# Kernel optimization log

Measured on AMD Instinct MI355X. Metric: run time of the kernel, lower is better.

## Reference

```python
import jax, jax.numpy as jnp
import numpy as np


def _skew(v):
    # v: [B,3] -> [B,3,3] skew-symmetric matrices
    z = jnp.zeros_like(v[:, 0])
    return jnp.stack([
        jnp.stack([z, -v[:, 2], v[:, 1]], axis=-1),
        jnp.stack([v[:, 2], z, -v[:, 0]], axis=-1),
        jnp.stack([-v[:, 1], v[:, 0], z], axis=-1),
    ], axis=-2)


def _so3_exp(phi):
    # phi: [B,3] -> [B,3,3] rotation matrices via Rodrigues formula
    theta_sq = jnp.sum(phi * phi, axis=-1)            # [B]
    small = theta_sq < 1e-8
    theta_sq_safe = jnp.where(small, 1.0, theta_sq)
    theta = jnp.sqrt(theta_sq_safe)
    A = jnp.where(small, 1.0 - theta_sq / 6.0, jnp.sin(theta) / theta)
    Bc = jnp.where(small, 0.5 - theta_sq / 24.0, (1.0 - jnp.cos(theta)) / theta_sq_safe)
    K = _skew(phi)                                    # [B,3,3]
    I = jnp.eye(3, dtype=phi.dtype)
    return I + A[:, None, None] * K + Bc[:, None, None] * (K @ K)


def setup_inputs() -> dict:
    key = jax.random.key(0)
    k1, = jax.random.split(key, 1)
    B, T = 4096, 1024
    imu = jax.random.normal(k1, (B, 6, T), dtype=jnp.float32) * 0.5  # gyro + accel
    t = jnp.broadcast_to(jnp.arange(T, dtype=jnp.float32) * 0.005, (B, T))  # 200 Hz
    x = jnp.concatenate([t[:, None, :], imu], axis=1)  # [B,7,T]
    return {"x": x}


def reference(x) -> jnp.ndarray:
    # x: [B,7,T] -> y: [B,15] = [DC (9), DV (3), DR (3)] per window
    Bn = x.shape[0]
    t = x[:, 0, :]                          # [B,T]
    dt = (t[:, 1:] - t[:, :-1]).T           # [T-1,B]
    w = jnp.moveaxis(x[:, 1:4, :-1], 2, 0)  # [T-1,B,3] gyro at idx-1
    a = jnp.moveaxis(x[:, 4:7, :-1], 2, 0)  # [T-1,B,3] accel at idx-1

    DC0 = jnp.broadcast_to(jnp.eye(3, dtype=x.dtype), (Bn, 3, 3))
    DV0 = jnp.zeros((Bn, 3), dtype=x.dtype)
    DR0 = jnp.zeros((Bn, 3), dtype=x.dtype)

    def step(carry, inp):
        DC, DV, DR = carry
        dt_k, w_k, a_k = inp                         # [B], [B,3], [B,3]
        dtc = dt_k[:, None]
        DCa = jnp.einsum('bij,bj->bi', DC, a_k)      # [B,3]
        DR = DR + DV * dtc + 0.5 * DCa * dtc * dtc
        DV = DV + DCa * dtc
        DC = DC @ _so3_exp(w_k * dtc)
        return (DC, DV, DR), None

    (DC, DV, DR), _ = jax.lax.scan(step, (DC0, DV0, DR0), (dt, w, a))
    return jnp.concatenate([DC.reshape(Bn, 9), DV, DR], axis=-1)  # [B,15]
```

## Files before the change

kernel.cpp:

```cpp
#include <hip/hip_runtime.h>

#define T_LEN 1024
#define NSTEP 1023

__device__ __forceinline__ void so3_exp(float px, float py, float pz, float R[9]) {
    float t2 = px * px + py * py + pz * pz;
    float A, Bc;
    if (t2 < 1e-2f) {
        float t4 = t2 * t2;
        A  = 1.0f - t2 * (1.0f / 6.0f)  + t4 * (1.0f / 120.0f);
        Bc = 0.5f - t2 * (1.0f / 24.0f) + t4 * (1.0f / 720.0f);
    } else {
        float th = sqrtf(t2);
        A = __sinf(th) / th;
        float sh = __sinf(0.5f * th);
        Bc = 2.0f * sh * sh / t2;
    }
    float xx = px * px, yy = py * py, zz = pz * pz;
    float xy = px * py, xz = px * pz, yz = py * pz;
    R[0] = 1.0f - Bc * (yy + zz);
    R[1] = Bc * xy - A * pz;
    R[2] = Bc * xz + A * py;
    R[3] = Bc * xy + A * pz;
    R[4] = 1.0f - Bc * (xx + zz);
    R[5] = Bc * yz - A * px;
    R[6] = Bc * xz - A * py;
    R[7] = Bc * yz + A * px;
    R[8] = 1.0f - Bc * (xx + yy);
}

extern "C" __global__ void __launch_bounds__(256)
rmi_kernel(const float* __restrict__ x, float* __restrict__ out) {
    const int b   = blockIdx.x;
    const int tid = threadIdx.x;
    const float* __restrict__ xb = x + (size_t)b * (7 * T_LEN);

    __shared__ float s[256 * 17];

    const int k0 = tid * 4;
    float4 t4  = *reinterpret_cast<const float4*>(xb + k0);
    float  tn  = (k0 + 4 < T_LEN) ? xb[k0 + 4] : 0.0f;
    float4 wx4 = *reinterpret_cast<const float4*>(xb + 1 * T_LEN + k0);
    float4 wy4 = *reinterpret_cast<const float4*>(xb + 2 * T_LEN + k0);
    float4 wz4 = *reinterpret_cast<const float4*>(xb + 3 * T_LEN + k0);
    float4 ax4 = *reinterpret_cast<const float4*>(xb + 4 * T_LEN + k0);
    float4 ay4 = *reinterpret_cast<const float4*>(xb + 5 * T_LEN + k0);
    float4 az4 = *reinterpret_cast<const float4*>(xb + 6 * T_LEN + k0);

    float tv[5]  = {t4.x, t4.y, t4.z, t4.w, tn};
    float wxv[4] = {wx4.x, wx4.y, wx4.z, wx4.w};
    float wyv[4] = {wy4.x, wy4.y, wy4.z, wy4.w};
    float wzv[4] = {wz4.x, wz4.y, wz4.z, wz4.w};
    float axv[4] = {ax4.x, ax4.y, ax4.z, ax4.w};
    float ayv[4] = {ay4.x, ay4.y, ay4.z, ay4.w};
    float azv[4] = {az4.x, az4.y, az4.z, az4.w};

    float C0 = 1.f, C1 = 0.f, C2 = 0.f;
    float C3 = 0.f, C4 = 1.f, C5 = 0.f;
    float C6 = 0.f, C7 = 0.f, C8 = 1.f;
    float V0 = 0.f, V1 = 0.f, V2 = 0.f;
    float R0 = 0.f, R1 = 0.f, R2 = 0.f;
    float tau = 0.f;

#pragma unroll
    for (int j = 0; j < 4; ++j) {
        int k = k0 + j;
        if (k < NSTEP) {
            float dt = tv[j + 1] - tv[j];
            float ax = axv[j], ay = ayv[j], az = azv[j];
            float Ca0 = C0 * ax + C1 * ay + C2 * az;
            float Ca1 = C3 * ax + C4 * ay + C5 * az;
            float Ca2 = C6 * ax + C7 * ay + C8 * az;
            float h = 0.5f * dt * dt;
            R0 += V0 * dt + Ca0 * h;
            R1 += V1 * dt + Ca1 * h;
            R2 += V2 * dt + Ca2 * h;
            V0 += Ca0 * dt;
            V1 += Ca1 * dt;
            V2 += Ca2 * dt;
            float Rk[9];
            so3_exp(wxv[j] * dt, wyv[j] * dt, wzv[j] * dt, Rk);
            float n0 = C0 * Rk[0] + C1 * Rk[3] + C2 * Rk[6];
            float n1 = C0 * Rk[1] + C1 * Rk[4] + C2 * Rk[7];
            float n2 = C0 * Rk[2] + C1 * Rk[5] + C2 * Rk[8];
            float n3 = C3 * Rk[0] + C4 * Rk[3] + C5 * Rk[6];
            float n4 = C3 * Rk[1] + C4 * Rk[4] + C5 * Rk[7];
            float n5 = C3 * Rk[2] + C4 * Rk[5] + C5 * Rk[8];
            float n6 = C6 * Rk[0] + C7 * Rk[3] + C8 * Rk[6];
            float n7 = C6 * Rk[1] + C7 * Rk[4] + C8 * Rk[7];
            float n8 = C6 * Rk[2] + C7 * Rk[5] + C8 * Rk[8];
            C0 = n0; C1 = n1; C2 = n2;
            C3 = n3; C4 = n4; C5 = n5;
            C6 = n6; C7 = n7; C8 = n8;
            tau += dt;
        }
    }

    float* me = s + tid * 17;
    me[0] = C0; me[1] = C1; me[2] = C2;
    me[3] = C3; me[4] = C4; me[5] = C5;
    me[6] = C6; me[7] = C7; me[8] = C8;
    me[9]  = V0; me[10] = V1; me[11] = V2;
    me[12] = R0; me[13] = R1; me[14] = R2;
    me[15] = tau;

    for (int str = 1; str < 256; str <<= 1) {
        __syncthreads();
        if ((tid & (2 * str - 1)) == 0) {
            const float* o = s + (tid + str) * 17;
            float M0 = o[0], M1 = o[1], M2 = o[2];
            float M3 = o[3], M4 = o[4], M5 = o[5];
            float M6 = o[6], M7 = o[7], M8 = o[8];
            float v0 = o[9], v1 = o[10], v2 = o[11];
            float r0 = o[12], r1 = o[13], r2 = o[14];
            float t2s = o[15];
            float nr0 = R0 + V0 * t2s + C0 * r0 + C1 * r1 + C2 * r2;
            float nr1 = R1 + V1 * t2s + C3 * r0 + C4 * r1 + C5 * r2;
            float nr2 = R2 + V2 * t2s + C6 * r0 + C7 * r1 + C8 * r2;
            float nv0 = V0 + C0 * v0 + C1 * v1 + C2 * v2;
            float nv1 = V1 + C3 * v0 + C4 * v1 + C5 * v2;
            float nv2 = V2 + C6 * v0 + C7 * v1 + C8 * v2;
            float n0 = C0 * M0 + C1 * M3 + C2 * M6;
            float n1 = C0 * M1 + C1 * M4 + C2 * M7;
            float n2 = C0 * M2 + C1 * M5 + C2 * M8;
            float n3 = C3 * M0 + C4 * M3 + C5 * M6;
            float n4 = C3 * M1 + C4 * M4 + C5 * M7;
            float n5 = C3 * M2 + C4 * M5 + C5 * M8;
            float n6 = C6 * M0 + C7 * M3 + C8 * M6;
            float n7 = C6 * M1 + C7 * M4 + C8 * M7;
            float n8 = C6 * M2 + C7 * M5 + C8 * M8;
            C0 = n0; C1 = n1; C2 = n2;
            C3 = n3; C4 = n4; C5 = n5;
            C6 = n6; C7 = n7; C8 = n8;
            V0 = nv0; V1 = nv1; V2 = nv2;
            R0 = nr0; R1 = nr1; R2 = nr2;
            tau += t2s;
            me[0] = C0; me[1] = C1; me[2] = C2;
            me[3] = C3; me[4] = C4; me[5] = C5;
            me[6] = C6; me[7] = C7; me[8] = C8;
            me[9]  = V0; me[10] = V1; me[11] = V2;
            me[12] = R0; me[13] = R1; me[14] = R2;
            me[15] = tau;
        }
    }

    if (tid == 0) {
        float* ob = out + (size_t)b * 15;
        ob[0] = C0; ob[1] = C1; ob[2] = C2;
        ob[3] = C3; ob[4] = C4; ob[5] = C5;
        ob[6] = C6; ob[7] = C7; ob[8] = C8;
        ob[9]  = V0; ob[10] = V1; ob[11] = V2;
        ob[12] = R0; ob[13] = R1; ob[14] = R2;
    }
}

extern "C" void kernel_launch(void* const* d_in, const int* in_sizes, int n_in,
                              void* d_out, int out_size, void* d_ws, size_t ws_size,
                              hipStream_t stream) {
    const float* x = (const float*)d_in[0];
    float* out = (float*)d_out;
    const int B = in_sizes[0] / (7 * T_LEN);
    rmi_kernel<<<B, 256, 0, stream>>>(x, out);
}
```

Baseline: 168.7 us.

## Map one window per wavefront with 16 steps per lane and shuffle reduction

Each 64-lane wavefront now processes one batch window, with every lane running 16 sequential steps instead of 4, and four windows share each 256-thread block. The shared-memory tree reduction with block-wide barriers is replaced by a wavefront shuffle reduction that composes the 16-float segment state. This removes the LDS traffic and __syncthreads steps of the old reduction, and the serial part per lane gets longer. Per-lane global loads are now strided by 64 bytes across lanes, which may reduce load coalescing.

```diff
diff --git a/kernel.cpp b/kernel.cpp
--- a/kernel.cpp
+++ b/kernel.cpp
@@ -2,155 +2,163 @@
 
 #define T_LEN 1024
 #define NSTEP 1023
+#define SPT   16
+
+struct El {
+    float c0,c1,c2,c3,c4,c5,c6,c7,c8;
+    float v0,v1,v2;
+    float r0,r1,r2;
+    float tau;
+};
+
+__device__ __forceinline__ El compose(const El& a, const El& b) {
+    El o;
+    o.r0 = a.r0 + a.v0*b.tau + a.c0*b.r0 + a.c1*b.r1 + a.c2*b.r2;
+    o.r1 = a.r1 + a.v1*b.tau + a.c3*b.r0 + a.c4*b.r1 + a.c5*b.r2;
+    o.r2 = a.r2 + a.v2*b.tau + a.c6*b.r0 + a.c7*b.r1 + a.c8*b.r2;
+    o.v0 = a.v0 + a.c0*b.v0 + a.c1*b.v1 + a.c2*b.v2;
+    o.v1 = a.v1 + a.c3*b.v0 + a.c4*b.v1 + a.c5*b.v2;
+    o.v2 = a.v2 + a.c6*b.v0 + a.c7*b.v1 + a.c8*b.v2;
+    o.c0 = a.c0*b.c0 + a.c1*b.c3 + a.c2*b.c6;
+    o.c1 = a.c0*b.c1 + a.c1*b.c4 + a.c2*b.c7;
+    o.c2 = a.c0*b.c2 + a.c1*b.c5 + a.c2*b.c8;
+    o.c3 = a.c3*b.c0 + a.c4*b.c3 + a.c5*b.c6;
+    o.c4 = a.c3*b.c1 + a.c4*b.c4 + a.c5*b.c7;
+    o.c5 = a.c3*b.c2 + a.c4*b.c5 + a.c5*b.c8;
+    o.c6 = a.c6*b.c0 + a.c7*b.c3 + a.c8*b.c6;
+    o.c7 = a.c6*b.c1 + a.c7*b.c4 + a.c8*b.c7;
+    o.c8 = a.c6*b.c2 + a.c7*b.c5 + a.c8*b.c8;
+    o.tau = a.tau + b.tau;
+    return o;
+}
+
+__device__ __forceinline__ El shfl_down_el(const El& e, int delta) {
+    El o;
+    o.c0 = __shfl_down(e.c0, delta);
+    o.c1 = __shfl_down(e.c1, delta);
+    o.c2 = __shfl_down(e.c2, delta);
+    o.c3 = __shfl_down(e.c3, delta);
+    o.c4 = __shfl_down(e.c4, delta);
+    o.c5 = __shfl_down(e.c5, delta);
+    o.c6 = __shfl_down(e.c6, delta);
+    o.c7 = __shfl_down(e.c7, delta);
+    o.c8 = __shfl_down(e.c8, delta);
+    o.v0 = __shfl_down(e.v0, delta);
+    o.v1 = __shfl_down(e.v1, delta);
+    o.v2 = __shfl_down(e.v2, delta);
+    o.r0 = __shfl_down(e.r0, delta);
+    o.r1 = __shfl_down(e.r1, delta);
+    o.r2 = __shfl_down(e.r2, delta);
+    o.tau = __shfl_down(e.tau, delta);
+    return o;
+}
 
 __device__ __forceinline__ void so3_exp(float px, float py, float pz, float R[9]) {
-    float t2 = px * px + py * py + pz * pz;
+    float t2 = px*px + py*py + pz*pz;
     float A, Bc;
     if (t2 < 1e-2f) {
-        float t4 = t2 * t2;
-        A  = 1.0f - t2 * (1.0f / 6.0f)  + t4 * (1.0f / 120.0f);
-        Bc = 0.5f - t2 * (1.0f / 24.0f) + t4 * (1.0f / 720.0f);
+        float t4 = t2*t2;
+        A  = 1.0f - t2*(1.0f/6.0f)  + t4*(1.0f/120.0f);
+        Bc = 0.5f - t2*(1.0f/24.0f) + t4*(1.0f/720.0f);
     } else {
         float th = sqrtf(t2);
-        A = __sinf(th) / th;
-        float sh = __sinf(0.5f * th);
-        Bc = 2.0f * sh * sh / t2;
+        A = __sinf(th)/th;
+        float sh = __sinf(0.5f*th);
+        Bc = 2.0f*sh*sh/t2;
     }
-    float xx = px * px, yy = py * py, zz = pz * pz;
-    float xy = px * py, xz = px * pz, yz = py * pz;
-    R[0] = 1.0f - Bc * (yy + zz);
-    R[1] = Bc * xy - A * pz;
-    R[2] = Bc * xz + A * py;
-    R[3] = Bc * xy + A * pz;
-    R[4] = 1.0f - Bc * (xx + zz);
-    R[5] = Bc * yz - A * px;
-    R[6] = Bc * xz - A * py;
-    R[7] = Bc * yz + A * px;
-    R[8] = 1.0f - Bc * (xx + yy);
+    float xx = px*px, yy = py*py, zz = pz*pz;
+    float xy = px*py, xz = px*pz, yz = py*pz;
+    R[0] = 1.0f - Bc*(yy+zz);
+    R[1] = Bc*xy - A*pz;
+    R[2] = Bc*xz + A*py;
+    R[3] = Bc*xy + A*pz;
+    R[4] = 1.0f - Bc*(xx+zz);
+    R[5] = Bc*yz - A*px;
+    R[6] = Bc*xz - A*py;
+    R[7] = Bc*yz + A*px;
+    R[8] = 1.0f - Bc*(xx+yy);
 }
 
 extern "C" __global__ void __launch_bounds__(256)
-rmi_kernel(const float* __restrict__ x, float* __restrict__ out) {
-    const int b   = blockIdx.x;
-    const int tid = threadIdx.x;
+rmi_kernel(const float* __restrict__ x, float* __restrict__ out, int B) {
+    const int lane = threadIdx.x & 63;
+    const int wid  = threadIdx.x >> 6;
+    const int b    = blockIdx.x * 4 + wid;
+    if (b >= B) return;
     const float* __restrict__ xb = x + (size_t)b * (7 * T_LEN);
+    const int k0 = lane * SPT;
 
-    __shared__ float s[256 * 17];
-
-    const int k0 = tid * 4;
-    float4 t4  = *reinterpret_cast<const float4*>(xb + k0);
-    float  tn  = (k0 + 4 < T_LEN) ? xb[k0 + 4] : 0.0f;
-    float4 wx4 = *reinterpret_cast<const float4*>(xb + 1 * T_LEN + k0);
-    float4 wy4 = *reinterpret_cast<const float4*>(xb + 2 * T_LEN + k0);
-    float4 wz4 = *reinterpret_cast<const float4*>(xb + 3 * T_LEN + k0);
-    float4 ax4 = *reinterpret_cast<const float4*>(xb + 4 * T_LEN + k0);
-    float4 ay4 = *reinterpret_cast<const float4*>(xb + 5 * T_LEN + k0);
-    float4 az4 = *reinterpret_cast<const float4*>(xb + 6 * T_LEN + k0);
-
-    float tv[5]  = {t4.x, t4.y, t4.z, t4.w, tn};
-    float wxv[4] = {wx4.x, wx4.y, wx4.z, wx4.w};
-    float wyv[4] = {wy4.x, wy4.y, wy4.z, wy4.w};
-    float wzv[4] = {wz4.x, wz4.y, wz4.z, wz4.w};
-    float axv[4] = {ax4.x, ax4.y, ax4.z, ax4.w};
-    float ayv[4] = {ay4.x, ay4.y, ay4.z, ay4.w};
-    float azv[4] = {az4.x, az4.y, az4.z, az4.w};
-
-    float C0 = 1.f, C1 = 0.f, C2 = 0.f;
-    float C3 = 0.f, C4 = 1.f, C5 = 0.f;
-    float C6 = 0.f, C7 = 0.f, C8 = 1.f;
-    float V0 = 0.f, V1 = 0.f, V2 = 0.f;
-    float R0 = 0.f, R1 = 0.f, R2 = 0.f;
-    float tau = 0.f;
+    El e = {1.f,0.f,0.f, 0.f,1.f,0.f, 0.f,0.f,1.f,
+            0.f,0.f,0.f, 0.f,0.f,0.f, 0.f};
 
 #pragma unroll
-    for (int j = 0; j < 4; ++j) {
-        int k = k0 + j;
-        if (k < NSTEP) {
-            float dt = tv[j + 1] - tv[j];
-            float ax = axv[j], ay = ayv[j], az = azv[j];
-            float Ca0 = C0 * ax + C1 * ay + C2 * az;
-            float Ca1 = C3 * ax + C4 * ay + C5 * az;
-            float Ca2 = C6 * ax + C7 * ay + C8 * az;
-            float h = 0.5f * dt * dt;
-            R0 += V0 * dt + Ca0 * h;
-            R1 += V1 * dt + Ca1 * h;
-            R2 += V2 * dt + Ca2 * h;
-            V0 += Ca0 * dt;
-            V1 += Ca1 * dt;
-            V2 += Ca2 * dt;
-            float Rk[9];
-            so3_exp(wxv[j] * dt, wyv[j] * dt, wzv[j] * dt, Rk);
-            float n0 = C0 * Rk[0] + C1 * Rk[3] + C2 * Rk[6];
-            float n1 = C0 * Rk[1] + C1 * Rk[4] + C2 * Rk[7];
-            float n2 = C0 * Rk[2] + C1 * Rk[5] + C2 * Rk[8];
-            float n3 = C3 * Rk[0] + C4 * Rk[3] + C5 * Rk[6];
-            float n4 = C3 * Rk[1] + C4 * Rk[4] + C5 * Rk[7];
-            float n5 = C3 * Rk[2] + C4 * Rk[5] + C5 * Rk[8];
-            float n6 = C6 * Rk[0] + C7 * Rk[3] + C8 * Rk[6];
-            float n7 = C6 * Rk[1] + C7 * Rk[4] + C8 * Rk[7];
-            float n8 = C6 * Rk[2] + C7 * Rk[5] + C8 * Rk[8];
-            C0 = n0; C1 = n1; C2 = n2;
-            C3 = n3; C4 = n4; C5 = n5;
-            C6 = n6; C7 = n7; C8 = n8;
-            tau += dt;
+    for (int c = 0; c < SPT/4; ++c) {
+        const int kc = k0 + 4*c;
+        float4 t4  = *reinterpret_cast<const float4*>(xb + kc);
+        float  tn  = (kc + 4 < T_LEN) ? xb[kc + 4] : 0.0f;
+        float4 wx4 = *reinterpret_cast<const float4*>(xb + 1*T_LEN + kc);
+        float4 wy4 = *reinterpret_cast<const float4*>(xb + 2*T_LEN + kc);
+        float4 wz4 = *reinterpret_cast<const float4*>(xb + 3*T_LEN + kc);
+        float4 ax4 = *reinterpret_cast<const float4*>(xb + 4*T_LEN + kc);
+        float4 ay4 = *reinterpret_cast<const float4*>(xb + 5*T_LEN + kc);
+        float4 az4 = *reinterpret_cast<const float4*>(xb + 6*T_LEN + kc);
+
+        float tv[5]  = {t4.x, t4.y, t4.z, t4.w, tn};
+        float wxv[4] = {wx4.x, wx4.y, wx4.z, wx4.w};
+        float wyv[4] = {wy4.x, wy4.y, wy4.z, wy4.w};
+        float wzv[4] = {wz4.x, wz4.y, wz4.z, wz4.w};
+        float axv[4] = {ax4.x, ax4.y, ax4.z, ax4.w};
+        float ayv[4] = {ay4.x, ay4.y, ay4.z, ay4.w};
+        float azv[4] = {az4.x, az4.y, az4.z, az4.w};
+
+#pragma unroll
+        for (int j = 0; j < 4; ++j) {
+            const int k = kc + j;
+            if (k < NSTEP) {
+                float dt = tv[j+1] - tv[j];
+                float ax = axv[j], ay = ayv[j], az = azv[j];
+                float Ca0 = e.c0*ax + e.c1*ay + e.c2*az;
+                float Ca1 = e.c3*ax + e.c4*ay + e.c5*az;
+                float Ca2 = e.c6*ax + e.c7*ay + e.c8*az;
+                float h = 0.5f * dt * dt;
+                e.r0 += e.v0*dt + Ca0*h;
+                e.r1 += e.v1*dt + Ca1*h;
+                e.r2 += e.v2*dt + Ca2*h;
+                e.v0 += Ca0*dt;
+                e.v1 += Ca1*dt;
+                e.v2 += Ca2*dt;
+                float Rk[9];
+                so3_exp(wxv[j]*dt, wyv[j]*dt, wzv[j]*dt, Rk);
+                float n0 = e.c0*Rk[0] + e.c1*Rk[3] + e.c2*Rk[6];
+                float n1 = e.c0*Rk[1] + e.c1*Rk[4] + e.c2*Rk[7];
+                float n2 = e.c0*Rk[2] + e.c1*Rk[5] + e.c2*Rk[8];
+                float n3 = e.c3*Rk[0] + e.c4*Rk[3] + e.c5*Rk[6];
+                float n4 = e.c3*Rk[1] + e.c4*Rk[4] + e.c5*Rk[7];
+                float n5 = e.c3*Rk[2] + e.c4*Rk[5] + e.c5*Rk[8];
+                float n6 = e.c6*Rk[0] + e.c7*Rk[3] + e.c8*Rk[6];
+                float n7 = e.c6*Rk[1] + e.c7*Rk[4] + e.c8*Rk[7];
+                float n8 = e.c6*Rk[2] + e.c7*Rk[5] + e.c8*Rk[8];
+                e.c0=n0; e.c1=n1; e.c2=n2;
+                e.c3=n3; e.c4=n4; e.c5=n5;
+                e.c6=n6; e.c7=n7; e.c8=n8;
+                e.tau += dt;
+            }
         }
     }
 
-    float* me = s + tid * 17;
-    me[0] = C0; me[1] = C1; me[2] = C2;
-    me[3] = C3; me[4] = C4; me[5] = C5;
-    me[6] = C6; me[7] = C7; me[8] = C8;
-    me[9]  = V0; me[10] = V1; me[11] = V2;
-    me[12] = R0; me[13] = R1; me[14] = R2;
-    me[15] = tau;
-
-    for (int str = 1; str < 256; str <<= 1) {
-        __syncthreads();
-        if ((tid & (2 * str - 1)) == 0) {
-            const float* o = s + (tid + str) * 17;
-            float M0 = o[0], M1 = o[1], M2 = o[2];
-            float M3 = o[3], M4 = o[4], M5 = o[5];
-            float M6 = o[6], M7 = o[7], M8 = o[8];
-            float v0 = o[9], v1 = o[10], v2 = o[11];
-            float r0 = o[12], r1 = o[13], r2 = o[14];
-            float t2s = o[15];
-            float nr0 = R0 + V0 * t2s + C0 * r0 + C1 * r1 + C2 * r2;
-            float nr1 = R1 + V1 * t2s + C3 * r0 + C4 * r1 + C5 * r2;
-            float nr2 = R2 + V2 * t2s + C6 * r0 + C7 * r1 + C8 * r2;
-            float nv0 = V0 + C0 * v0 + C1 * v1 + C2 * v2;
-            float nv1 = V1 + C3 * v0 + C4 * v1 + C5 * v2;
-            float nv2 = V2 + C6 * v0 + C7 * v1 + C8 * v2;
-            float n0 = C0 * M0 + C1 * M3 + C2 * M6;
-            float n1 = C0 * M1 + C1 * M4 + C2 * M7;
-            float n2 = C0 * M2 + C1 * M5 + C2 * M8;
-            float n3 = C3 * M0 + C4 * M3 + C5 * M6;
-            float n4 = C3 * M1 + C4 * M4 + C5 * M7;
-            float n5 = C3 * M2 + C4 * M5 + C5 * M8;
-            float n6 = C6 * M0 + C7 * M3 + C8 * M6;
-            float n7 = C6 * M1 + C7 * M4 + C8 * M7;
-            float n8 = C6 * M2 + C7 * M5 + C8 * M8;
-            C0 = n0; C1 = n1; C2 = n2;
-            C3 = n3; C4 = n4; C5 = n5;
-            C6 = n6; C7 = n7; C8 = n8;
-            V0 = nv0; V1 = nv1; V2 = nv2;
-            R0 = nr0; R1 = nr1; R2 = nr2;
-            tau += t2s;
-            me[0] = C0; me[1] = C1; me[2] = C2;
-            me[3] = C3; me[4] = C4; me[5] = C5;
-            me[6] = C6; me[7] = C7; me[8] = C8;
-            me[9]  = V0; me[10] = V1; me[11] = V2;
-            me[12] = R0; me[13] = R1; me[14] = R2;
-            me[15] = tau;
-        }
+#pragma unroll
+    for (int str = 1; str < 64; str <<= 1) {
+        El o = shfl_down_el(e, str);
+        e = compose(e, o);
     }
 
-    if (tid == 0) {
+    if (lane == 0) {
         float* ob = out + (size_t)b * 15;
-        ob[0] = C0; ob[1] = C1; ob[2] = C2;
-        ob[3] = C3; ob[4] = C4; ob[5] = C5;
-        ob[6] = C6; ob[7] = C7; ob[8] = C8;
-        ob[9]  = V0; ob[10] = V1; ob[11] = V2;
-        ob[12] = R0; ob[13] = R1; ob[14] = R2;
+        ob[0]=e.c0;  ob[1]=e.c1;  ob[2]=e.c2;
+        ob[3]=e.c3;  ob[4]=e.c4;  ob[5]=e.c5;
+        ob[6]=e.c6;  ob[7]=e.c7;  ob[8]=e.c8;
+        ob[9]=e.v0;  ob[10]=e.v1; ob[11]=e.v2;
+        ob[12]=e.r0; ob[13]=e.r1; ob[14]=e.r2;
     }
 }
 
@@ -160,5 +168,5 @@
     const float* x = (const float*)d_in[0];
     float* out = (float*)d_out;
     const int B = in_sizes[0] / (7 * T_LEN);
-    rmi_kernel<<<B, 256, 0, stream>>>(x, out);
+    rmi_kernel<<<(B + 3) / 4, 256, 0, stream>>>(x, out, B);
 }
```

After: 179.6 us. 1.06x slower.
